# Kernel tuning notes

Measured on AMD Instinct MI355X. Metric: run time of the kernel, lower is better.

The kernel has to match this reference:

```python
import jax, jax.numpy as jnp
import numpy as np

T, H, I, E, K = 4096, 2048, 1408, 8, 2


def setup_inputs() -> dict:
    key = jax.random.key(0)
    k1, k2, k3, k4, k5, k6 = jax.random.split(key, 6)
    hidden_states = jax.random.normal(k1, (T, H), dtype=jnp.float32)
    top_k_index = jax.random.randint(k2, (T, K), 0, E, dtype=jnp.int32)
    top_k_weights = jax.random.uniform(k3, (T, K), dtype=jnp.float32)
    # nn.Linear stores weight as [out_features, in_features]
    s_h = 1.0 / np.sqrt(H)
    s_i = 1.0 / np.sqrt(I)
    gate_w = jax.random.uniform(k4, (E, I, H), dtype=jnp.float32, minval=-s_h, maxval=s_h)
    up_w = jax.random.uniform(k5, (E, I, H), dtype=jnp.float32, minval=-s_h, maxval=s_h)
    down_w = jax.random.uniform(k6, (E, H, I), dtype=jnp.float32, minval=-s_i, maxval=s_i)
    return {
        "hidden_states": hidden_states,
        "top_k_index": top_k_index,
        "top_k_weights": top_k_weights,
        "gate_w": gate_w,
        "up_w": up_w,
        "down_w": down_w,
    }


def reference(hidden_states, top_k_index, top_k_weights, gate_w, up_w, down_w):
    # combine[t, e] = sum_k top_k_weights[t, k] * 1[top_k_index[t, k] == e]
    num_experts = gate_w.shape[0]
    one_hot = jax.nn.one_hot(top_k_index, num_experts, dtype=hidden_states.dtype)  # [T, K, E]
    combine = jnp.einsum("tk,tke->te", top_k_weights, one_hot)  # [T, E]

    # dense-equivalent of per-expert gather -> SwiGLU MLP -> scatter-add
    gate = jnp.einsum("th,eih->tei", hidden_states, gate_w)  # [T, E, I]
    up = jnp.einsum("th,eih->tei", hidden_states, up_w)      # [T, E, I]
    inter = jax.nn.silu(gate) * up                               # [T, E, I]
    out = jnp.einsum("te,tei,ehi->th", combine, inter, down_w)  # [T, H]
    return out
```

## Files before the change

### kernel.cpp

```cpp
#include <hip/hip_runtime.h>
#include <cstdint>
#include <cstddef>

#define T_TOK 4096
#define HD 2048
#define ID 1408
#define NE 8
#define NA (T_TOK * 2)
#define MAXR 10240
#define MAXT 40
#define EIH ((size_t)NE * ID * HD)
#define N4 ((int)(EIH / 4))
#define NCGU 2048
#define NCASTD 512
#define NTILE_G (MAXR / 256)
#define NGEMM_GU (NTILE_G * (ID / 128))
#define NKGU (HD / 64)
#define NKD  (ID / 64)

typedef __bf16 bf16x8 __attribute__((ext_vector_type(8)));
typedef float f32x4 __attribute__((ext_vector_type(4)));

#define MFMA16 __builtin_amdgcn_mfma_f32_16x16x32_bf16
#define LD8(base, off) (*(const bf16x8*)&(base)[(off)])

__device__ __forceinline__ unsigned short f2bf(float f) {
  union { float f; unsigned int u; } c; c.f = f;
  unsigned int u = c.u;
  u += 0x7fffu + ((u >> 16) & 1u);
  return (unsigned short)(u >> 16);
}

__device__ __forceinline__ void gl_lds16(const unsigned short* g, unsigned short* l) {
  __builtin_amdgcn_global_load_lds(
      (const __attribute__((address_space(1))) unsigned int*)g,
      (__attribute__((address_space(3))) unsigned int*)l, 16, 0, 0);
}

__device__ __forceinline__ int swz_off(int R, int fq) {
  int q = ((R & 1) << 2) | fq;
  int p = q ^ ((R >> 1) & 7);
  return (R >> 1) * 64 + p * 8;
}
__device__ __forceinline__ int lds_off(int ks, int P, int fq) {
  return ks * 8192 + swz_off(P, fq);
}

__global__ void moe_count(const int* __restrict__ idx, int* __restrict__ cnt) {
  int a = blockIdx.x * 256 + threadIdx.x;
  if (a < NA) atomicAdd(&cnt[idx[a]], 1);
}

__global__ void moe_scan(const int* __restrict__ cnt, int* __restrict__ seg,
                         int* __restrict__ work_e, int* __restrict__ work_r,
                         int* __restrict__ ntiles) {
  if (blockIdx.x == 0 && threadIdx.x == 0) {
    int off = 0, nt = 0;
    for (int e = 0; e < NE; ++e) {
      seg[e] = off;
      int c = cnt[e];
      int tiles = (c + 255) >> 8;
      for (int tb = 0; tb < tiles; ++tb) {
        work_e[nt] = e;
        work_r[nt] = off + tb * 256;
        ++nt;
      }
      off += tiles << 8;
    }
    *ntiles = nt;
  }
}

__global__ void moe_fill(const int* __restrict__ idx, const float* __restrict__ wts,
                         const int* __restrict__ seg, int* __restrict__ cnt2,
                         int* __restrict__ row_token, float* __restrict__ row_weight,
                         int* __restrict__ slot_of) {
  int a = blockIdx.x * 256 + threadIdx.x;
  if (a < NA) {
    int e = idx[a];
    int pos = atomicAdd(&cnt2[e], 1);
    int slot = seg[e] + pos;
    row_token[slot] = a >> 1;
    row_weight[slot] = wts[a];
    slot_of[a] = slot;
  }
}

__global__ void mega_gather_castgu(
    const float* __restrict__ hidden, const int* __restrict__ slot_of,
    unsigned short* __restrict__ Xg,
    const float* __restrict__ gate_w, const float* __restrict__ up_w,
    unsigned short* __restrict__ gate_bf, unsigned short* __restrict__ ub_out) {
  const int bx = blockIdx.x;
  if (bx < NA) {
    const int slot = slot_of[bx];
    const int t = bx >> 1;
    const float4* src = (const float4*)(hidden + (size_t)t * HD);
    ushort4* dst = (ushort4*)(Xg + (size_t)slot * HD);
#pragma unroll
    for (int j = 0; j < 2; ++j) {
      int i = threadIdx.x + j * 256;
      float4 v = src[i];
      ushort4 o;
      o.x = f2bf(v.x); o.y = f2bf(v.y); o.z = f2bf(v.z); o.w = f2bf(v.w);
      dst[i] = o;
    }
  } else {
    const int cb = bx - NA;
    const int total = 2 * N4;
    for (int i = cb * 256 + threadIdx.x; i < total; i += NCGU * 256) {
      const float* s; unsigned short* t; int j = i;
      if (j < N4) { s = gate_w; t = gate_bf; }
      else { s = up_w; t = ub_out; j -= N4; }
      f32x4 v = __builtin_nontemporal_load((const f32x4*)s + j);
      ushort4 o;
      o.x = f2bf(v[0]); o.y = f2bf(v[1]); o.z = f2bf(v[2]); o.w = f2bf(v[3]);
      ((ushort4*)t)[j] = o;
    }
  }
}

__global__ __launch_bounds__(512, 2) void moe_gateup(
    const unsigned short* __restrict__ Xg,
    const unsigned short* __restrict__ Wg,
    const unsigned short* __restrict__ Wu,
    unsigned short* __restrict__ inter,
    const int* __restrict__ work_e, const int* __restrict__ work_r,
    const int* __restrict__ ntiles,
    const float* __restrict__ down_w, unsigned short* __restrict__ down_bf) {
  const int bx = blockIdx.x;
  if (bx >= NGEMM_GU) {
    const int cb = bx - NGEMM_GU;
    for (int i = cb * 512 + threadIdx.x; i < N4; i += NCASTD * 512) {
      f32x4 v = __builtin_nontemporal_load((const f32x4*)down_w + i);
      ushort4 o;
      o.x = f2bf(v[0]); o.y = f2bf(v[1]); o.z = f2bf(v[2]); o.w = f2bf(v[3]);
      ((ushort4*)down_bf)[i] = o;
    }
    return;
  }
  const int g = (bx & 7) * (NGEMM_GU / 8) + (bx >> 3);
  const int tile = g % NTILE_G;
  if (tile >= *ntiles) return;
  const int e = work_e[tile];
  const int row0 = work_r[tile];
  const int col0 = (g / NTILE_G) * 128;

  __shared__ unsigned short As[2][16384];
  __shared__ unsigned short Bs[2][16384];

  const int tid = threadIdx.x;
  const int lane = tid & 63;
  const int wave = tid >> 6;
  const int wm = wave >> 2, wn = wave & 3;
  const int p_l = lane & 7;
  const int ub  = lane >> 3;
  const int q_l = p_l ^ ub;
  const int srow = (ub << 1) | (q_l >> 2);
  const int scol = (q_l & 3) << 3;
  const int fm = lane & 15, fq = lane >> 4;

  const size_t a_base = (size_t)row0 * HD;
  const size_t b_base = ((size_t)e * ID + col0) * HD;

  f32x4 zero = {0.f, 0.f, 0.f, 0.f};
  f32x4 accg[8][2], accu[8][2];
#pragma unroll
  for (int mi = 0; mi < 8; ++mi)
#pragma unroll
    for (int j = 0; j < 2; ++j) { accg[mi][j] = zero; accu[mi][j] = zero; }

  auto stA = [&](int k0, int b, int h) {
    const int abase = ((wave >> 2) << 7) + (h << 6) + ((wave & 3) << 4);
    const int pp = (h << 7) + (wave << 4);
#pragma unroll
    for (int s = 0; s < 2; ++s)
      gl_lds16(Xg + a_base + (size_t)(abase + srow) * HD + k0 + s * 32 + scol,
               &As[b][s * 8192 + pp * 32]);
  };
  auto stB = [&](int k0, int b, int h) {
    const unsigned short* W = h ? Wu : Wg;
    const int pp = (h << 7) + (wave << 4);
#pragma unroll
    for (int s = 0; s < 2; ++s)
      gl_lds16(W + b_base + (size_t)((wave << 4) + srow) * HD + k0 + s * 32 + scol,
               &Bs[b][s * 8192 + pp * 32]);
  };

  stA(0, 0, 0); stB(0, 0, 0); stB(0, 0, 1); stA(0, 0, 1);
  asm volatile("s_waitcnt vmcnt(4)" ::: "memory");
  __builtin_amdgcn_s_barrier();

  bf16x8 a[4][2], bg[2][2], bu[2][2];
#pragma unroll 1
  for (int t = 0; t < NKGU; ++t) {
    const int k1 = (t + 1) << 6;
    const bool pf = (t + 1 < NKGU);
    const unsigned short* Ab = As[t & 1];
    const unsigned short* Bb = Bs[t & 1];
    const int bn = (t & 1) ^ 1;

#pragma unroll
    for (int i = 0; i < 4; ++i)
#pragma unroll
      for (int ks = 0; ks < 2; ++ks)
        a[i][ks] = LD8(Ab, lds_off(ks, wm * 64 + i * 16 + fm, fq));
#pragma unroll
    for (int j = 0; j < 2; ++j)
#pragma unroll
      for (int ks = 0; ks < 2; ++ks)
        bg[j][ks] = LD8(Bb, lds_off(ks, wn * 32 + j * 16 + fm, fq));
    if (pf) stA(k1, bn, 0);
    __builtin_amdgcn_s_barrier();
    asm volatile("s_waitcnt lgkmcnt(0)" ::: "memory");
    __builtin_amdgcn_sched_barrier(0);
    __builtin_amdgcn_s_setprio(1);
#pragma unroll
    for (int mi = 0; mi < 4; ++mi)
#pragma unroll
      for (int j = 0; j < 2; ++j)
#pragma unroll
        for (int ks = 0; ks < 2; ++ks)
          accg[mi][j] = MFMA16(a[mi][ks], bg[j][ks], accg[mi][j], 0, 0, 0);
    __builtin_amdgcn_s_setprio(0);
    if (pf) asm volatile("s_waitcnt vmcnt(4)" ::: "memory");
    else    asm volatile("s_waitcnt vmcnt(2)" ::: "memory");
    __builtin_amdgcn_s_barrier();

#pragma unroll
    for (int j = 0; j < 2; ++j)
#pragma unroll
      for (int ks = 0; ks < 2; ++ks)
        bu[j][ks] = LD8(Bb, lds_off(ks, 128 + wn * 32 + j * 16 + fm, fq));
    if (pf) stB(k1, bn, 0);
    __builtin_amdgcn_s_barrier();
    asm volatile("s_waitcnt lgkmcnt(0)" ::: "memory");
    __builtin_amdgcn_sched_barrier(0);
    __builtin_amdgcn_s_setprio(1);
#pragma unroll
    for (int mi = 0; mi < 4; ++mi)
#pragma unroll
      for (int j = 0; j < 2; ++j)
#pragma unroll
        for (int ks = 0; ks < 2; ++ks)
          accu[mi][j] = MFMA16(a[mi][ks], bu[j][ks], accu[mi][j], 0, 0, 0);
    __builtin_amdgcn_s_setprio(0);
    if (pf) asm volatile("s_waitcnt vmcnt(4)" ::: "memory");
    else    asm volatile("s_waitcnt vmcnt(0)" ::: "memory");
    __builtin_amdgcn_s_barrier();

#pragma unroll
    for (int i = 0; i < 4; ++i)
#pragma unroll
      for (int ks = 0; ks < 2; ++ks)
        a[i][ks] = LD8(Ab, lds_off(ks, 128 + wm * 64 + i * 16 + fm, fq));
    if (pf) stB(k1, bn, 1);
    __builtin_amdgcn_s_barrier();
    asm volatile("s_waitcnt lgkmcnt(0)" ::: "memory");
    __builtin_amdgcn_sched_barrier(0);
    __builtin_amdgcn_s_setprio(1);
#pragma unroll
    for (int mi = 0; mi < 4; ++mi)
#pragma unroll
      for (int j = 0; j < 2; ++j)
#pragma unroll
        for (int ks = 0; ks < 2; ++ks)
          accu[4 + mi][j] = MFMA16(a[mi][ks], bu[j][ks], accu[4 + mi][j], 0, 0, 0);
    __builtin_amdgcn_s_setprio(0);
    __builtin_amdgcn_s_barrier();

    if (pf) stA(k1, bn, 1);
    __builtin_amdgcn_s_barrier();
    __builtin_amdgcn_s_setprio(1);
#pragma unroll
    for (int mi = 0; mi < 4; ++mi)
#pragma unroll
      for (int j = 0; j < 2; ++j)
#pragma unroll
        for (int ks = 0; ks < 2; ++ks)
          accg[4 + mi][j] = MFMA16(a[mi][ks], bg[j][ks], accg[4 + mi][j], 0, 0, 0);
    __builtin_amdgcn_s_setprio(0);
    if (pf) asm volatile("s_waitcnt vmcnt(4)" ::: "memory");
    __builtin_amdgcn_s_barrier();
  }

#pragma unroll
  for (int mi = 0; mi < 8; ++mi)
#pragma unroll
    for (int j = 0; j < 2; ++j)
#pragma unroll
      for (int r = 0; r < 4; ++r) {
        float gg = accg[mi][j][r];
        float u = accu[mi][j][r];
        float v = (gg / (1.0f + __expf(-gg))) * u;
        int row = row0 + wm * 128 + mi * 16 + fq * 4 + r;
        int col = col0 + wn * 32 + j * 16 + fm;
        inter[(size_t)row * ID + col] = f2bf(v);
      }
}

__global__ __launch_bounds__(512, 2) void moe_down(
    const unsigned short* __restrict__ inter,
    const unsigned short* __restrict__ Wd,
    float* __restrict__ out,
    const int* __restrict__ work_e, const int* __restrict__ work_r,
    const int* __restrict__ ntiles,
    const int* __restrict__ row_token, const float* __restrict__ row_weight) {
  const int tile = blockIdx.x;
  if (tile >= *ntiles) return;
  const int e = work_e[tile];
  const int row0 = work_r[tile];
  const int col0 = blockIdx.y * 256;

  __shared__ unsigned short As[2][16384];
  __shared__ unsigned short Bs[2][16384];
  __shared__ int tok_s[256];
  __shared__ float w_s[256];

  const int tid = threadIdx.x;
  if (tid < 256) {
    tok_s[tid] = row_token[row0 + tid];
    w_s[tid] = row_weight[row0 + tid];
  }

  const int lane = tid & 63;
  const int wave = tid >> 6;
  const int wm = wave >> 2, wn = wave & 3;
  const int p_l = lane & 7;
  const int ub  = lane >> 3;
  const int q_l = p_l ^ ub;
  const int srow = (ub << 1) | (q_l >> 2);
  const int scol = (q_l & 3) << 3;
  const int fm = lane & 15, fq = lane >> 4;

  const size_t a_base = (size_t)row0 * ID;
  const size_t b_base = ((size_t)e * HD + col0) * ID;

  f32x4 zero = {0.f, 0.f, 0.f, 0.f};
  f32x4 acc[8][4];
#pragma unroll
  for (int mi = 0; mi < 8; ++mi)
#pragma unroll
    for (int j = 0; j < 4; ++j) acc[mi][j] = zero;

  auto stA = [&](int k0, int b, int h) {
    const int abase = ((wave >> 2) << 7) + (h << 6) + ((wave & 3) << 4);
    const int pp = (h << 7) + (wave << 4);
#pragma unroll
    for (int s = 0; s < 2; ++s)
      gl_lds16(inter + a_base + (size_t)(abase + srow) * ID + k0 + s * 32 + scol,
               &As[b][s * 8192 + pp * 32]);
  };
  auto stB = [&](int k0, int b, int h) {
    const int bbase = ((wave >> 1) << 6) + (h << 5) + ((wave & 1) << 4);
    const int pp = (h << 7) + (wave << 4);
#pragma unroll
    for (int s = 0; s < 2; ++s)
      gl_lds16(Wd + b_base + (size_t)(bbase + srow) * ID + k0 + s * 32 + scol,
               &Bs[b][s * 8192 + pp * 32]);
  };

  stA(0, 0, 0); stB(0, 0, 0); stB(0, 0, 1); stA(0, 0, 1);
  asm volatile("s_waitcnt vmcnt(4)" ::: "memory");
  __builtin_amdgcn_s_barrier();

  bf16x8 a[4][2], b0[2][2], b1[2][2];
#pragma unroll 1
  for (int t = 0; t < NKD; ++t) {
    const int k1 = (t + 1) << 6;
    const bool pf = (t + 1 < NKD);
    const unsigned short* Ab = As[t & 1];
    const unsigned short* Bb = Bs[t & 1];
    const int bn = (t & 1) ^ 1;

#pragma unroll
    for (int i = 0; i < 4; ++i)
#pragma unroll
      for (int ks = 0; ks < 2; ++ks)
        a[i][ks] = LD8(Ab, lds_off(ks, wm * 64 + i * 16 + fm, fq));
#pragma unroll
    for (int j = 0; j < 2; ++j)
#pragma unroll
      for (int ks = 0; ks < 2; ++ks)
        b0[j][ks] = LD8(Bb, lds_off(ks, wn * 32 + j * 16 + fm, fq));
    if (pf) stA(k1, bn, 0);
    __builtin_amdgcn_s_barrier();
    asm volatile("s_waitcnt lgkmcnt(0)" ::: "memory");
    __builtin_amdgcn_sched_barrier(0);
    __builtin_amdgcn_s_setprio(1);
#pragma unroll
    for (int mi = 0; mi < 4; ++mi)
#pragma unroll
      for (int j = 0; j < 2; ++j)
#pragma unroll
        for (int ks = 0; ks < 2; ++ks)
          acc[mi][j] = MFMA16(a[mi][ks], b0[j][ks], acc[mi][j], 0, 0, 0);
    __builtin_amdgcn_s_setprio(0);
    if (pf) asm volatile("s_waitcnt vmcnt(4)" ::: "memory");
    else    asm volatile("s_waitcnt vmcnt(2)" ::: "memory");
    __builtin_amdgcn_s_barrier();

#pragma unroll
    for (int j = 0; j < 2; ++j)
#pragma unroll
      for (int ks = 0; ks < 2; ++ks)
        b1[j][ks] = LD8(Bb, lds_off(ks, 128 + wn * 32 + j * 16 + fm, fq));
    if (pf) stB(k1, bn, 0);
    __builtin_amdgcn_s_barrier();
    asm volatile("s_waitcnt lgkmcnt(0)" ::: "memory");
    __builtin_amdgcn_sched_barrier(0);
    __builtin_amdgcn_s_setprio(1);
#pragma unroll
    for (int mi = 0; mi < 4; ++mi)
#pragma unroll
      for (int j = 0; j < 2; ++j)
#pragma unroll
        for (int ks = 0; ks < 2; ++ks)
          acc[mi][2 + j] = MFMA16(a[mi][ks], b1[j][ks], acc[mi][2 + j], 0, 0, 0);
    __builtin_amdgcn_s_setprio(0);
    if (pf) asm volatile("s_waitcnt vmcnt(4)" ::: "memory");
    else    asm volatile("s_waitcnt vmcnt(0)" ::: "memory");
    __builtin_amdgcn_s_barrier();

#pragma unroll
    for (int i = 0; i < 4; ++i)
#pragma unroll
      for (int ks = 0; ks < 2; ++ks)
        a[i][ks] = LD8(Ab, lds_off(ks, 128 + wm * 64 + i * 16 + fm, fq));
    if (pf) stB(k1, bn, 1);
    __builtin_amdgcn_s_barrier();
    asm volatile("s_waitcnt lgkmcnt(0)" ::: "memory");
    __builtin_amdgcn_sched_barrier(0);
    __builtin_amdgcn_s_setprio(1);
#pragma unroll
    for (int mi = 0; mi < 4; ++mi)
#pragma unroll
      for (int j = 0; j < 2; ++j)
#pragma unroll
        for (int ks = 0; ks < 2; ++ks)
          acc[4 + mi][2 + j] = MFMA16(a[mi][ks], b1[j][ks], acc[4 + mi][2 + j], 0, 0, 0);
    __builtin_amdgcn_s_setprio(0);
    __builtin_amdgcn_s_barrier();

    if (pf) stA(k1, bn, 1);
    __builtin_amdgcn_s_barrier();
    __builtin_amdgcn_s_setprio(1);
#pragma unroll
    for (int mi = 0; mi < 4; ++mi)
#pragma unroll
      for (int j = 0; j < 2; ++j)
#pragma unroll
        for (int ks = 0; ks < 2; ++ks)
          acc[4 + mi][j] = MFMA16(a[mi][ks], b0[j][ks], acc[4 + mi][j], 0, 0, 0);
    __builtin_amdgcn_s_setprio(0);
    if (pf) asm volatile("s_waitcnt vmcnt(4)" ::: "memory");
    __builtin_amdgcn_s_barrier();
  }

#pragma unroll
  for (int mi = 0; mi < 8; ++mi)
#pragma unroll
    for (int j = 0; j < 4; ++j)
#pragma unroll
      for (int r = 0; r < 4; ++r) {
        int rl = wm * 128 + mi * 16 + fq * 4 + r;
        int tok = tok_s[rl];
        if (tok >= 0) {
          int col = col0 + wn * 64 + (j >> 1) * 32 + (j & 1) * 16 + fm;
          atomicAdd(&out[(size_t)tok * HD + col], w_s[rl] * acc[mi][j][r]);
        }
      }
}

extern "C" void kernel_launch(void* const* d_in, const int* in_sizes, int n_in,
                              void* d_out, int out_size, void* d_ws, size_t ws_size,
                              hipStream_t stream) {
  const float* hidden = (const float*)d_in[0];
  const int* topk_idx = (const int*)d_in[1];
  const float* topk_w = (const float*)d_in[2];
  const float* gate_w = (const float*)d_in[3];
  const float* up_w = (const float*)d_in[4];
  const float* down_w = (const float*)d_in[5];
  float* out = (float*)d_out;

  char* ws = (char*)d_ws;
  size_t o_gate = 0;
  size_t o_up   = o_gate + EIH * 2;
  size_t o_down = o_up + EIH * 2;
  size_t o_xg   = o_down + EIH * 2;
  size_t o_int  = o_xg + (size_t)MAXR * HD * 2;
  size_t o_tok  = o_int + (size_t)MAXR * ID * 2;
  size_t o_wgt  = o_tok + (size_t)MAXR * 4;
  size_t o_slot = o_wgt + (size_t)MAXR * 4;
  size_t o_small = o_slot + (size_t)NA * 4;

  unsigned short* gate_bf = (unsigned short*)(ws + o_gate);
  unsigned short* up_bf   = (unsigned short*)(ws + o_up);
  unsigned short* down_bf = (unsigned short*)(ws + o_down);
  unsigned short* Xg      = (unsigned short*)(ws + o_xg);
  unsigned short* inter   = (unsigned short*)(ws + o_int);
  int* row_token = (int*)(ws + o_tok);
  float* row_weight = (float*)(ws + o_wgt);
  int* slot_of = (int*)(ws + o_slot);
  int* cnt    = (int*)(ws + o_small);
  int* cnt2   = cnt + 8;
  int* seg    = cnt + 16;
  int* ntiles = cnt + 24;
  int* work_e = cnt + 32;
  int* work_r = cnt + 32 + MAXT;

  hipMemsetAsync(out, 0, (size_t)T_TOK * HD * 4, stream);
  hipMemsetAsync(cnt, 0, (32 + 2 * MAXT) * 4, stream);
  hipMemsetAsync(row_token, 0xFF, (size_t)MAXR * 4, stream);

  moe_count<<<NA / 256, 256, 0, stream>>>(topk_idx, cnt);
  moe_scan<<<1, 64, 0, stream>>>(cnt, seg, work_e, work_r, ntiles);
  moe_fill<<<NA / 256, 256, 0, stream>>>(topk_idx, topk_w, seg, cnt2,
                                         row_token, row_weight, slot_of);

  mega_gather_castgu<<<NA + NCGU, 256, 0, stream>>>(hidden, slot_of, Xg,
                                                    gate_w, up_w, gate_bf, up_bf);

  moe_gateup<<<NGEMM_GU + NCASTD, 512, 0, stream>>>(
      Xg, gate_bf, up_bf, inter, work_e, work_r, ntiles, down_w, down_bf);

  dim3 gridB(NTILE_G, HD / 256);
  moe_down<<<gridB, 512, 0, stream>>>(inter, down_bf, out, work_e, work_r, ntiles,
                                      row_token, row_weight);
}
```

Baseline: 620.6 us.

## Fuse fp32-to-bf16 casts and token gather into GEMM loads; single-block routing

New measurement: 769.2 us. 1.24x slower.

```diff
diff --git a/kernel.cpp b/kernel.cpp
--- a/kernel.cpp
+++ b/kernel.cpp
@@ -9,10 +9,6 @@
 #define NA (T_TOK * 2)
 #define MAXR 10240
 #define MAXT 40
-#define EIH ((size_t)NE * ID * HD)
-#define N4 ((int)(EIH / 4))
-#define NCGU 2048
-#define NCASTD 512
 #define NTILE_G (MAXR / 256)
 #define NGEMM_GU (NTILE_G * (ID / 128))
 #define NKGU (HD / 64)
@@ -31,6 +27,19 @@
   return (unsigned short)(u >> 16);
 }
 
+__device__ __forceinline__ unsigned int cvtpk(float lo, float hi) {
+  unsigned int r;
+  asm volatile("v_cvt_pk_bf16_f32 %0, %1, %2" : "=v"(r) : "v"(lo), "v"(hi));
+  return r;
+}
+
+__device__ __forceinline__ uint4 cvt8(const f32x4& v0, const f32x4& v1) {
+  uint4 w;
+  w.x = cvtpk(v0[0], v0[1]); w.y = cvtpk(v0[2], v0[3]);
+  w.z = cvtpk(v1[0], v1[1]); w.w = cvtpk(v1[2], v1[3]);
+  return w;
+}
+
 __device__ __forceinline__ void gl_lds16(const unsigned short* g, unsigned short* l) {
   __builtin_amdgcn_global_load_lds(
       (const __attribute__((address_space(1))) unsigned int*)g,
@@ -46,99 +55,55 @@
   return ks * 8192 + swz_off(P, fq);
 }
 
-__global__ void moe_count(const int* __restrict__ idx, int* __restrict__ cnt) {
-  int a = blockIdx.x * 256 + threadIdx.x;
-  if (a < NA) atomicAdd(&cnt[idx[a]], 1);
-}
-
-__global__ void moe_scan(const int* __restrict__ cnt, int* __restrict__ seg,
-                         int* __restrict__ work_e, int* __restrict__ work_r,
-                         int* __restrict__ ntiles) {
-  if (blockIdx.x == 0 && threadIdx.x == 0) {
+__global__ void moe_route(const int* __restrict__ idx, const float* __restrict__ wts,
+                          int* __restrict__ work_e, int* __restrict__ work_r,
+                          int* __restrict__ ntiles,
+                          int* __restrict__ row_token, float* __restrict__ row_weight) {
+  __shared__ int off_s[256 * 8];
+  __shared__ int seg_s[8];
+  __shared__ int cnt_s[8];
+  const int tid = threadIdx.x;
+  for (int i = tid; i < MAXR; i += 256) row_token[i] = -1;
+#pragma unroll
+  for (int e = 0; e < 8; ++e) off_s[tid * 8 + e] = 0;
+  const int a0 = tid * 32;
+  for (int j = 0; j < 32; ++j) off_s[tid * 8 + idx[a0 + j]]++;
+  __syncthreads();
+  if (tid < 8) {
+    int run = 0;
+    for (int t = 0; t < 256; ++t) {
+      int v = off_s[t * 8 + tid]; off_s[t * 8 + tid] = run; run += v;
+    }
+    cnt_s[tid] = run;
+  }
+  __syncthreads();
+  if (tid == 0) {
     int off = 0, nt = 0;
     for (int e = 0; e < NE; ++e) {
-      seg[e] = off;
-      int c = cnt[e];
-      int tiles = (c + 255) >> 8;
-      for (int tb = 0; tb < tiles; ++tb) {
-        work_e[nt] = e;
-        work_r[nt] = off + tb * 256;
-        ++nt;
-      }
+      seg_s[e] = off;
+      int tiles = (cnt_s[e] + 255) >> 8;
+      for (int tb = 0; tb < tiles; ++tb) { work_e[nt] = e; work_r[nt] = off + tb * 256; ++nt; }
       off += tiles << 8;
     }
     *ntiles = nt;
   }
-}
-
-__global__ void moe_fill(const int* __restrict__ idx, const float* __restrict__ wts,
-                         const int* __restrict__ seg, int* __restrict__ cnt2,
-                         int* __restrict__ row_token, float* __restrict__ row_weight,
-                         int* __restrict__ slot_of) {
-  int a = blockIdx.x * 256 + threadIdx.x;
-  if (a < NA) {
+  __syncthreads();
+  for (int j = 0; j < 32; ++j) {
+    int a = a0 + j;
     int e = idx[a];
-    int pos = atomicAdd(&cnt2[e], 1);
-    int slot = seg[e] + pos;
+    int slot = seg_s[e] + off_s[tid * 8 + e]++;
     row_token[slot] = a >> 1;
     row_weight[slot] = wts[a];
-    slot_of[a] = slot;
-  }
-}
-
-__global__ void mega_gather_castgu(
-    const float* __restrict__ hidden, const int* __restrict__ slot_of,
-    unsigned short* __restrict__ Xg,
-    const float* __restrict__ gate_w, const float* __restrict__ up_w,
-    unsigned short* __restrict__ gate_bf, unsigned short* __restrict__ ub_out) {
-  const int bx = blockIdx.x;
-  if (bx < NA) {
-    const int slot = slot_of[bx];
-    const int t = bx >> 1;
-    const float4* src = (const float4*)(hidden + (size_t)t * HD);
-    ushort4* dst = (ushort4*)(Xg + (size_t)slot * HD);
-#pragma unroll
-    for (int j = 0; j < 2; ++j) {
-      int i = threadIdx.x + j * 256;
-      float4 v = src[i];
-      ushort4 o;
-      o.x = f2bf(v.x); o.y = f2bf(v.y); o.z = f2bf(v.z); o.w = f2bf(v.w);
-      dst[i] = o;
-    }
-  } else {
-    const int cb = bx - NA;
-    const int total = 2 * N4;
-    for (int i = cb * 256 + threadIdx.x; i < total; i += NCGU * 256) {
-      const float* s; unsigned short* t; int j = i;
-      if (j < N4) { s = gate_w; t = gate_bf; }
-      else { s = up_w; t = ub_out; j -= N4; }
-      f32x4 v = __builtin_nontemporal_load((const f32x4*)s + j);
-      ushort4 o;
-      o.x = f2bf(v[0]); o.y = f2bf(v[1]); o.z = f2bf(v[2]); o.w = f2bf(v[3]);
-      ((ushort4*)t)[j] = o;
-    }
   }
 }
 
 __global__ __launch_bounds__(512, 2) void moe_gateup(
-    const unsigned short* __restrict__ Xg,
-    const unsigned short* __restrict__ Wg,
-    const unsigned short* __restrict__ Wu,
+    const float* __restrict__ hidden,
+    const float* __restrict__ Wg, const float* __restrict__ Wu,
     unsigned short* __restrict__ inter,
     const int* __restrict__ work_e, const int* __restrict__ work_r,
-    const int* __restrict__ ntiles,
-    const float* __restrict__ down_w, unsigned short* __restrict__ down_bf) {
+    const int* __restrict__ ntiles, const int* __restrict__ row_token) {
   const int bx = blockIdx.x;
-  if (bx >= NGEMM_GU) {
-    const int cb = bx - NGEMM_GU;
-    for (int i = cb * 512 + threadIdx.x; i < N4; i += NCASTD * 512) {
-      f32x4 v = __builtin_nontemporal_load((const f32x4*)down_w + i);
-      ushort4 o;
-      o.x = f2bf(v[0]); o.y = f2bf(v[1]); o.z = f2bf(v[2]); o.w = f2bf(v[3]);
-      ((ushort4*)down_bf)[i] = o;
-    }
-    return;
-  }
   const int g = (bx & 7) * (NGEMM_GU / 8) + (bx >> 3);
   const int tile = g % NTILE_G;
   if (tile >= *ntiles) return;
@@ -148,6 +113,7 @@
 
   __shared__ unsigned short As[2][16384];
   __shared__ unsigned short Bs[2][16384];
+  __shared__ int tok_s[256];
 
   const int tid = threadIdx.x;
   const int lane = tid & 63;
@@ -160,8 +126,57 @@
   const int scol = (q_l & 3) << 3;
   const int fm = lane & 15, fq = lane >> 4;
 
-  const size_t a_base = (size_t)row0 * HD;
+  if (tid < 256) { int tk = row_token[row0 + tid]; tok_s[tid] = tk < 0 ? 0 : tk; }
+  __syncthreads();
+
   const size_t b_base = ((size_t)e * ID + col0) * HD;
+  size_t rowAoff[2];
+#pragma unroll
+  for (int h = 0; h < 2; ++h) {
+    int r = ((wave >> 2) << 7) + (h << 6) + ((wave & 3) << 4) + srow;
+    rowAoff[h] = (size_t)tok_s[r] * HD;
+  }
+  const float* pB[2] = { Wg + b_base + (size_t)((wave << 4) + srow) * HD,
+                         Wu + b_base + (size_t)((wave << 4) + srow) * HD };
+
+  f32x4 rA[2][2][2], rB[2][2][2];
+
+  auto loadA = [&](int k0) {
+#pragma unroll
+    for (int h = 0; h < 2; ++h)
+#pragma unroll
+      for (int s = 0; s < 2; ++s)
+#pragma unroll
+        for (int p = 0; p < 2; ++p)
+          rA[h][s][p] = *(const f32x4*)(hidden + rowAoff[h] + k0 + s * 32 + scol + p * 4);
+  };
+  auto loadB = [&](int k0) {
+#pragma unroll
+    for (int h = 0; h < 2; ++h)
+#pragma unroll
+      for (int s = 0; s < 2; ++s)
+#pragma unroll
+        for (int p = 0; p < 2; ++p)
+          rB[h][s][p] = *(const f32x4*)(pB[h] + k0 + s * 32 + scol + p * 4);
+  };
+  auto writeA = [&](int b) {
+#pragma unroll
+    for (int h = 0; h < 2; ++h) {
+      const int pp = (h << 7) + (wave << 4);
+#pragma unroll
+      for (int s = 0; s < 2; ++s)
+        *(uint4*)&As[b][s * 8192 + pp * 32 + lane * 8] = cvt8(rA[h][s][0], rA[h][s][1]);
+    }
+  };
+  auto writeB = [&](int b) {
+#pragma unroll
+    for (int h = 0; h < 2; ++h) {
+      const int pp = (h << 7) + (wave << 4);
+#pragma unroll
+      for (int s = 0; s < 2; ++s)
+        *(uint4*)&Bs[b][s * 8192 + pp * 32 + lane * 8] = cvt8(rB[h][s][0], rB[h][s][1]);
+    }
+  };
 
   f32x4 zero = {0.f, 0.f, 0.f, 0.f};
   f32x4 accg[8][2], accu[8][2];
@@ -170,32 +185,19 @@
 #pragma unroll
     for (int j = 0; j < 2; ++j) { accg[mi][j] = zero; accu[mi][j] = zero; }
 
-  auto stA = [&](int k0, int b, int h) {
-    const int abase = ((wave >> 2) << 7) + (h << 6) + ((wave & 3) << 4);
-    const int pp = (h << 7) + (wave << 4);
-#pragma unroll
-    for (int s = 0; s < 2; ++s)
-      gl_lds16(Xg + a_base + (size_t)(abase + srow) * HD + k0 + s * 32 + scol,
-               &As[b][s * 8192 + pp * 32]);
-  };
-  auto stB = [&](int k0, int b, int h) {
-    const unsigned short* W = h ? Wu : Wg;
-    const int pp = (h << 7) + (wave << 4);
-#pragma unroll
-    for (int s = 0; s < 2; ++s)
-      gl_lds16(W + b_base + (size_t)((wave << 4) + srow) * HD + k0 + s * 32 + scol,
-               &Bs[b][s * 8192 + pp * 32]);
-  };
-
-  stA(0, 0, 0); stB(0, 0, 0); stB(0, 0, 1); stA(0, 0, 1);
-  asm volatile("s_waitcnt vmcnt(4)" ::: "memory");
+  loadA(0); loadB(0);
+  asm volatile("s_waitcnt vmcnt(0)" ::: "memory");
+  writeA(0); writeB(0);
+  loadA(64); loadB(64);
+  asm volatile("s_waitcnt lgkmcnt(0)" ::: "memory");
   __builtin_amdgcn_s_barrier();
 
   bf16x8 a[4][2], bg[2][2], bu[2][2];
 #pragma unroll 1
   for (int t = 0; t < NKGU; ++t) {
-    const int k1 = (t + 1) << 6;
+    const int k2 = (t + 2) << 6;
     const bool pf = (t + 1 < NKGU);
+    const bool pf2 = (t + 2 < NKGU);
     const unsigned short* Ab = As[t & 1];
     const unsigned short* Bb = Bs[t & 1];
     const int bn = (t & 1) ^ 1;
@@ -210,7 +212,11 @@
 #pragma unroll
       for (int ks = 0; ks < 2; ++ks)
         bg[j][ks] = LD8(Bb, lds_off(ks, wn * 32 + j * 16 + fm, fq));
-    if (pf) stA(k1, bn, 0);
+    if (pf) {
+      asm volatile("s_waitcnt vmcnt(8)" ::: "memory");
+      writeA(bn);
+      if (pf2) loadA(k2);
+    }
     __builtin_amdgcn_s_barrier();
     asm volatile("s_waitcnt lgkmcnt(0)" ::: "memory");
     __builtin_amdgcn_sched_barrier(0);
@@ -223,8 +229,6 @@
         for (int ks = 0; ks < 2; ++ks)
           accg[mi][j] = MFMA16(a[mi][ks], bg[j][ks], accg[mi][j], 0, 0, 0);
     __builtin_amdgcn_s_setprio(0);
-    if (pf) asm volatile("s_waitcnt vmcnt(4)" ::: "memory");
-    else    asm volatile("s_waitcnt vmcnt(2)" ::: "memory");
     __builtin_amdgcn_s_barrier();
 
 #pragma unroll
@@ -232,7 +236,6 @@
 #pragma unroll
       for (int ks = 0; ks < 2; ++ks)
         bu[j][ks] = LD8(Bb, lds_off(ks, 128 + wn * 32 + j * 16 + fm, fq));
-    if (pf) stB(k1, bn, 0);
     __builtin_amdgcn_s_barrier();
     asm volatile("s_waitcnt lgkmcnt(0)" ::: "memory");
     __builtin_amdgcn_sched_barrier(0);
@@ -245,8 +248,6 @@
         for (int ks = 0; ks < 2; ++ks)
           accu[mi][j] = MFMA16(a[mi][ks], bu[j][ks], accu[mi][j], 0, 0, 0);
     __builtin_amdgcn_s_setprio(0);
-    if (pf) asm volatile("s_waitcnt vmcnt(4)" ::: "memory");
-    else    asm volatile("s_waitcnt vmcnt(0)" ::: "memory");
     __builtin_amdgcn_s_barrier();
 
 #pragma unroll
@@ -254,7 +255,12 @@
 #pragma unroll
       for (int ks = 0; ks < 2; ++ks)
         a[i][ks] = LD8(Ab, lds_off(ks, 128 + wm * 64 + i * 16 + fm, fq));
-    if (pf) stB(k1, bn, 1);
+    if (pf) {
+      if (pf2) asm volatile("s_waitcnt vmcnt(8)" ::: "memory");
+      else     asm volatile("s_waitcnt vmcnt(0)" ::: "memory");
+      writeB(bn);
+      if (pf2) loadB(k2);
+    }
     __builtin_amdgcn_s_barrier();
     asm volatile("s_waitcnt lgkmcnt(0)" ::: "memory");
     __builtin_amdgcn_sched_barrier(0);
@@ -269,8 +275,6 @@
     __builtin_amdgcn_s_setprio(0);
     __builtin_amdgcn_s_barrier();
 
-    if (pf) stA(k1, bn, 1);
-    __builtin_amdgcn_s_barrier();
     __builtin_amdgcn_s_setprio(1);
 #pragma unroll
     for (int mi = 0; mi < 4; ++mi)
@@ -280,7 +284,6 @@
         for (int ks = 0; ks < 2; ++ks)
           accg[4 + mi][j] = MFMA16(a[mi][ks], bg[j][ks], accg[4 + mi][j], 0, 0, 0);
     __builtin_amdgcn_s_setprio(0);
-    if (pf) asm volatile("s_waitcnt vmcnt(4)" ::: "memory");
     __builtin_amdgcn_s_barrier();
   }
 
@@ -301,7 +304,7 @@
 
 __global__ __launch_bounds__(512, 2) void moe_down(
     const unsigned short* __restrict__ inter,
-    const unsigned short* __restrict__ Wd,
+    const float* __restrict__ Wd,
     float* __restrict__ out,
     const int* __restrict__ work_e, const int* __restrict__ work_r,
     const int* __restrict__ ntiles,
@@ -322,6 +325,7 @@
     tok_s[tid] = row_token[row0 + tid];
     w_s[tid] = row_weight[row0 + tid];
   }
+  __syncthreads();
 
   const int lane = tid & 63;
   const int wave = tid >> 6;
@@ -336,6 +340,45 @@
   const size_t a_base = (size_t)row0 * ID;
   const size_t b_base = ((size_t)e * HD + col0) * ID;
 
+  const float* pBd[2];
+#pragma unroll
+  for (int h = 0; h < 2; ++h) {
+    int bbase = ((wave >> 1) << 6) + (h << 5) + ((wave & 1) << 4);
+    pBd[h] = Wd + b_base + (size_t)(bbase + srow) * ID;
+  }
+
+  f32x4 rB[2][2][2];
+
+  auto stA = [&](int k0, int b) {
+#pragma unroll
+    for (int h = 0; h < 2; ++h) {
+      const int abase = ((wave >> 2) << 7) + (h << 6) + ((wave & 3) << 4);
+      const int pp = (h << 7) + (wave << 4);
+#pragma unroll
+      for (int s = 0; s < 2; ++s)
+        gl_lds16(inter + a_base + (size_t)(abase + srow) * ID + k0 + s * 32 + scol,
+                 &As[b][s * 8192 + pp * 32]);
+    }
+  };
+  auto loadB = [&](int k0) {
+#pragma unroll
+    for (int h = 0; h < 2; ++h)
+#pragma unroll
+      for (int s = 0; s < 2; ++s)
+#pragma unroll
+        for (int p = 0; p < 2; ++p)
+          rB[h][s][p] = *(const f32x4*)(pBd[h] + k0 + s * 32 + scol + p * 4);
+  };
+  auto writeB = [&](int b) {
+#pragma unroll
+    for (int h = 0; h < 2; ++h) {
+      const int pp = (h << 7) + (wave << 4);
+#pragma unroll
+      for (int s = 0; s < 2; ++s)
+        *(uint4*)&Bs[b][s * 8192 + pp * 32 + lane * 8] = cvt8(rB[h][s][0], rB[h][s][1]);
+    }
+  };
+
   f32x4 zero = {0.f, 0.f, 0.f, 0.f};
   f32x4 acc[8][4];
 #pragma unroll
@@ -343,32 +386,21 @@
 #pragma unroll
     for (int j = 0; j < 4; ++j) acc[mi][j] = zero;
 
-  auto stA = [&](int k0, int b, int h) {
-    const int abase = ((wave >> 2) << 7) + (h << 6) + ((wave & 3) << 4);
-    const int pp = (h << 7) + (wave << 4);
-#pragma unroll
-    for (int s = 0; s < 2; ++s)
-      gl_lds16(inter + a_base + (size_t)(abase + srow) * ID + k0 + s * 32 + scol,
-               &As[b][s * 8192 + pp * 32]);
-  };
-  auto stB = [&](int k0, int b, int h) {
-    const int bbase = ((wave >> 1) << 6) + (h << 5) + ((wave & 1) << 4);
-    const int pp = (h << 7) + (wave << 4);
-#pragma unroll
-    for (int s = 0; s < 2; ++s)
-      gl_lds16(Wd + b_base + (size_t)(bbase + srow) * ID + k0 + s * 32 + scol,
-               &Bs[b][s * 8192 + pp * 32]);
-  };
-
-  stA(0, 0, 0); stB(0, 0, 0); stB(0, 0, 1); stA(0, 0, 1);
-  asm volatile("s_waitcnt vmcnt(4)" ::: "memory");
+  loadB(0);
+  stA(0, 0);
+  asm volatile("s_waitcnt vmcnt(0)" ::: "memory");
+  writeB(0);
+  loadB(64);
+  asm volatile("s_waitcnt lgkmcnt(0)" ::: "memory");
   __builtin_amdgcn_s_barrier();
 
   bf16x8 a[4][2], b0[2][2], b1[2][2];
 #pragma unroll 1
   for (int t = 0; t < NKD; ++t) {
     const int k1 = (t + 1) << 6;
+    const int k2 = (t + 2) << 6;
     const bool pf = (t + 1 < NKD);
+    const bool pf2 = (t + 2 < NKD);
     const unsigned short* Ab = As[t & 1];
     const unsigned short* Bb = Bs[t & 1];
     const int bn = (t & 1) ^ 1;
@@ -383,7 +415,7 @@
 #pragma unroll
       for (int ks = 0; ks < 2; ++ks)
         b0[j][ks] = LD8(Bb, lds_off(ks, wn * 32 + j * 16 + fm, fq));
-    if (pf) stA(k1, bn, 0);
+    if (pf) stA(k1, bn);
     __builtin_amdgcn_s_barrier();
     asm volatile("s_waitcnt lgkmcnt(0)" ::: "memory");
     __builtin_amdgcn_sched_barrier(0);
@@ -396,8 +428,6 @@
         for (int ks = 0; ks < 2; ++ks)
           acc[mi][j] = MFMA16(a[mi][ks], b0[j][ks], acc[mi][j], 0, 0, 0);
     __builtin_amdgcn_s_setprio(0);
-    if (pf) asm volatile("s_waitcnt vmcnt(4)" ::: "memory");
-    else    asm volatile("s_waitcnt vmcnt(2)" ::: "memory");
     __builtin_amdgcn_s_barrier();
 
 #pragma unroll
@@ -405,7 +435,6 @@
 #pragma unroll
       for (int ks = 0; ks < 2; ++ks)
         b1[j][ks] = LD8(Bb, lds_off(ks, 128 + wn * 32 + j * 16 + fm, fq));
-    if (pf) stB(k1, bn, 0);
     __builtin_amdgcn_s_barrier();
     asm volatile("s_waitcnt lgkmcnt(0)" ::: "memory");
     __builtin_amdgcn_sched_barrier(0);
@@ -418,8 +447,6 @@
         for (int ks = 0; ks < 2; ++ks)
           acc[mi][2 + j] = MFMA16(a[mi][ks], b1[j][ks], acc[mi][2 + j], 0, 0, 0);
     __builtin_amdgcn_s_setprio(0);
-    if (pf) asm volatile("s_waitcnt vmcnt(4)" ::: "memory");
-    else    asm volatile("s_waitcnt vmcnt(0)" ::: "memory");
     __builtin_amdgcn_s_barrier();
 
 #pragma unroll
@@ -427,7 +454,11 @@
 #pragma unroll
       for (int ks = 0; ks < 2; ++ks)
         a[i][ks] = LD8(Ab, lds_off(ks, 128 + wm * 64 + i * 16 + fm, fq));
-    if (pf) stB(k1, bn, 1);
+    if (pf) {
+      asm volatile("s_waitcnt vmcnt(4)" ::: "memory");
+      writeB(bn);
+      if (pf2) loadB(k2);
+    }
     __builtin_amdgcn_s_barrier();
     asm volatile("s_waitcnt lgkmcnt(0)" ::: "memory");
     __builtin_amdgcn_sched_barrier(0);
@@ -442,8 +473,6 @@
     __builtin_amdgcn_s_setprio(0);
     __builtin_amdgcn_s_barrier();
 
-    if (pf) stA(k1, bn, 1);
-    __builtin_amdgcn_s_barrier();
     __builtin_amdgcn_s_setprio(1);
 #pragma unroll
     for (int mi = 0; mi < 4; ++mi)
@@ -453,7 +482,10 @@
         for (int ks = 0; ks < 2; ++ks)
           acc[4 + mi][j] = MFMA16(a[mi][ks], b0[j][ks], acc[4 + mi][j], 0, 0, 0);
     __builtin_amdgcn_s_setprio(0);
-    if (pf) asm volatile("s_waitcnt vmcnt(4)" ::: "memory");
+    if (pf) {
+      if (pf2) asm volatile("s_waitcnt vmcnt(8)" ::: "memory");
+      else     asm volatile("s_waitcnt vmcnt(0)" ::: "memory");
+    }
     __builtin_amdgcn_s_barrier();
   }
 
@@ -484,47 +516,27 @@
   float* out = (float*)d_out;
 
   char* ws = (char*)d_ws;
-  size_t o_gate = 0;
-  size_t o_up   = o_gate + EIH * 2;
-  size_t o_down = o_up + EIH * 2;
-  size_t o_xg   = o_down + EIH * 2;
-  size_t o_int  = o_xg + (size_t)MAXR * HD * 2;
-  size_t o_tok  = o_int + (size_t)MAXR * ID * 2;
-  size_t o_wgt  = o_tok + (size_t)MAXR * 4;
-  size_t o_slot = o_wgt + (size_t)MAXR * 4;
-  size_t o_small = o_slot + (size_t)NA * 4;
-
-  unsigned short* gate_bf = (unsigned short*)(ws + o_gate);
-  unsigned short* up_bf   = (unsigned short*)(ws + o_up);
-  unsigned short* down_bf = (unsigned short*)(ws + o_down);
-  unsigned short* Xg      = (unsigned short*)(ws + o_xg);
-  unsigned short* inter   = (unsigned short*)(ws + o_int);
+  size_t o_int = 0;
+  size_t o_tok = o_int + (size_t)MAXR * ID * 2;
+  size_t o_wgt = o_tok + (size_t)MAXR * 4;
+  size_t o_wrk = o_wgt + (size_t)MAXR * 4;
+
+  unsigned short* inter = (unsigned short*)(ws + o_int);
   int* row_token = (int*)(ws + o_tok);
   float* row_weight = (float*)(ws + o_wgt);
-  int* slot_of = (int*)(ws + o_slot);
-  int* cnt    = (int*)(ws + o_small);
-  int* cnt2   = cnt + 8;
-  int* seg    = cnt + 16;
-  int* ntiles = cnt + 24;
-  int* work_e = cnt + 32;
-  int* work_r = cnt + 32 + MAXT;
+  int* work_e = (int*)(ws + o_wrk);
+  int* work_r = work_e + MAXT;
+  int* ntiles = work_r + MAXT;
 
   hipMemsetAsync(out, 0, (size_t)T_TOK * HD * 4, stream);
-  hipMemsetAsync(cnt, 0, (32 + 2 * MAXT) * 4, stream);
-  hipMemsetAsync(row_token, 0xFF, (size_t)MAXR * 4, stream);
-
-  moe_count<<<NA / 256, 256, 0, stream>>>(topk_idx, cnt);
-  moe_scan<<<1, 64, 0, stream>>>(cnt, seg, work_e, work_r, ntiles);
-  moe_fill<<<NA / 256, 256, 0, stream>>>(topk_idx, topk_w, seg, cnt2,
-                                         row_token, row_weight, slot_of);
-
-  mega_gather_castgu<<<NA + NCGU, 256, 0, stream>>>(hidden, slot_of, Xg,
-                                                    gate_w, up_w, gate_bf, up_bf);
-
-  moe_gateup<<<NGEMM_GU + NCASTD, 512, 0, stream>>>(
-      Xg, gate_bf, up_bf, inter, work_e, work_r, ntiles, down_w, down_bf);
+
+  moe_route<<<1, 256, 0, stream>>>(topk_idx, topk_w, work_e, work_r, ntiles,
+                                   row_token, row_weight);
+
+  moe_gateup<<<NGEMM_GU, 512, 0, stream>>>(
+      hidden, gate_w, up_w, inter, work_e, work_r, ntiles, row_token);
 
   dim3 gridB(NTILE_G, HD / 256);
-  moe_down<<<gridB, 512, 0, stream>>>(inter, down_bf, out, work_e, work_r, ntiles,
+  moe_down<<<gridB, 512, 0, stream>>>(inter, down_w, out, work_e, work_r, ntiles,
                                       row_token, row_weight);
 }
```
